# Performance work log

Measured on AMD Instinct MI355X. Metric: run time of the kernel, lower is better.

## Reference

```python
import jax, jax.numpy as jnp
from jax import lax
import numpy as np

B, N, T = 16, 1024, 12
H_DIM, D_FF, NHEADS = 64, 256, 4
SDIM, DDIM, WDIM = 32, 16, 15
D_IN = 1 + SDIM + DDIM + WDIM  # 64


def setup_inputs() -> dict:
    key = jax.random.key(0)
    ks = jax.random.split(key, 32)
    def p(k, shape, s=0.05):
        return jax.random.normal(k, shape, dtype=jnp.float32) * s
    h = H_DIM
    inp = {
        'flow': jax.random.normal(ks[0], (B, N, T), dtype=jnp.float32),
        'day_idx': jax.random.randint(ks[1], (B, N, T), 0, 288),
        'week_idx': jax.random.randint(ks[2], (B, N, T), 0, 7),
        'spatial_emb': p(ks[3], (N, SDIM)),
        'daily_emb': p(ks[4], (288, DDIM)),
        'weekly_emb': p(ks[5], (7, WDIM)),
        'gfs_fc_w': p(ks[6], (h, D_IN)), 'gfs_fc_b': jnp.zeros(h),
        'glu_w': p(ks[7], (2 * h, h)), 'glu_b': jnp.zeros(2 * h),
        'gc_weight': p(ks[8], (h, h)),
        'gc_A': p(ks[9], (N, N), 0.02), 'gc_A2': p(ks[10], (N, N), 0.02),
        'ds_init_w': p(ks[11], (2 * h, h, 1, 3)), 'ds_init_b': jnp.zeros(2 * h),
        'ds_p1m_w': p(ks[12], (h, h, 1, 3)), 'ds_p1m_b': jnp.zeros(h),
        'ds_p1g_w': p(ks[13], (h, h, 1, 3)), 'ds_p1g_b': jnp.zeros(h),
        'ds_p2m_w': p(ks[14], (h, h, 1, 3)), 'ds_p2m_b': jnp.zeros(h),
        'ds_p2g_w': p(ks[15], (h, h, 1, 3)), 'ds_p2g_b': jnp.zeros(h),
        'ds_fc_w': p(ks[16], (h, 2 * h)), 'ds_fc_b': jnp.zeros(h),
        'wq': p(ks[17], (h, h)), 'bq': jnp.zeros(h),
        'wk': p(ks[18], (h, h)), 'bk': jnp.zeros(h),
        'wv': p(ks[19], (h, h)), 'bv': jnp.zeros(h),
        'wo': p(ks[20], (h, h)), 'bo': jnp.zeros(h),
        'ff1_w': p(ks[21], (D_FF, h)), 'ff1_b': jnp.zeros(D_FF),
        'ff2_w': p(ks[22], (h, D_FF)), 'ff2_b': jnp.zeros(h),
        'ln1_g': jnp.ones(h), 'ln1_b': jnp.zeros(h),
        'ln2_g': jnp.ones(h), 'ln2_b': jnp.zeros(h),
        'cl_w': p(ks[23], (T,)), 'cl_b': jnp.zeros(()),
    }
    return inp


def _ln(x, g, b):
    m = jnp.mean(x, -1, keepdims=True)
    v = jnp.mean(jnp.square(x - m), -1, keepdims=True)
    return (x - m) * lax.rsqrt(v + 1e-5) * g + b


def _conv1xk(x, w, b):
    # x: [B, C, N, T], w: [O, I, 1, 3], padding (0,1) along time
    y = lax.conv_general_dilated(x, w, (1, 1), ((0, 0), (1, 1)),
                                 dimension_numbers=('NCHW', 'OIHW', 'NCHW'))
    return y + b[None, :, None, None]


def reference(flow, day_idx, week_idx, spatial_emb, daily_emb, weekly_emb,
              gfs_fc_w, gfs_fc_b, glu_w, glu_b, gc_weight, gc_A, gc_A2,
              ds_init_w, ds_init_b, ds_p1m_w, ds_p1m_b, ds_p1g_w, ds_p1g_b,
              ds_p2m_w, ds_p2m_b, ds_p2g_w, ds_p2g_b, ds_fc_w, ds_fc_b,
              wq, bq, wk, bk, wv, bv, wo, bo, ff1_w, ff1_b, ff2_w, ff2_b,
              ln1_g, ln1_b, ln2_g, ln2_b, cl_w, cl_b):
    h = H_DIM
    # --- InfoEmb: concat flow + spatial + daily + weekly embeddings ---
    sp = jnp.broadcast_to(spatial_emb[None, :, None, :], (B, N, T, SDIM))
    x = jnp.concatenate([flow[..., None], sp, daily_emb[day_idx], weekly_emb[week_idx]], -1)  # [B,N,T,64]
    # --- GFS: 1x1 conv + GLU (channels == last dim) ---
    x = x @ gfs_fc_w.T + gfs_fc_b
    g = x @ glu_w.T + glu_b
    lhs, rhs = g[..., :h], g[..., h:]
    x = lhs * jax.nn.sigmoid(rhs)  # [B,N,T,h]
    # --- TASTGC: adaptive spatial graph conv with two learned adjacencies ---
    A1 = jax.nn.softmax(jax.nn.relu(gc_A), axis=1)
    A2 = jax.nn.softmax(jax.nn.relu(gc_A2), axis=1)
    hs = jnp.einsum('mn,bntd->bmtd', A1, x) + jnp.einsum('mn,bntd->bmtd', A2, x)
    x = jax.nn.relu(jnp.einsum('bntd,de->bnte', hs, gc_weight))  # [B,N,T,h]
    # --- DSFIN: dual-path gated temporal conv ---
    xd = jnp.transpose(x, (0, 3, 1, 2))  # [B,h,N,T]
    x_init = _conv1xk(xd, ds_init_w, ds_init_b)  # [B,2h,N,T]
    p1, p2 = x_init[:, :h], x_init[:, h:]
    p1o = _conv1xk(p1, ds_p1m_w, ds_p1m_b) * jax.nn.sigmoid(_conv1xk(p1, ds_p1g_w, ds_p1g_b))
    p2o = _conv1xk(p2, ds_p2m_w, ds_p2m_b) * jax.nn.sigmoid(_conv1xk(p2, ds_p2g_w, ds_p2g_b))
    fused = jax.nn.relu(jnp.concatenate([p1o, p2o], 1) + x_init)  # [B,2h,N,T]
    fused = jnp.transpose(fused, (0, 2, 3, 1))  # [B,N,T,2h]
    x = fused @ ds_fc_w.T + ds_fc_b  # [B,N,T,h]
    # --- EncoderLayer: multi-head attention along time per node ---
    dk = h // NHEADS
    y = x.reshape(B * N, T, h)
    q = (y @ wq.T + bq).reshape(B * N, T, NHEADS, dk)
    k = (y @ wk.T + bk).reshape(B * N, T, NHEADS, dk)
    v = (y @ wv.T + bv).reshape(B * N, T, NHEADS, dk)
    scores = jnp.einsum('blhd,bshd->bhls', q, k) / jnp.sqrt(jnp.float32(dk))
    attn = jax.nn.softmax(scores, -1)
    o = jnp.einsum('bhls,bshd->blhd', attn, v).reshape(B * N, T, h)
    y1 = _ln(y + (o @ wo.T + bo), ln1_g, ln1_b)
    ff = jax.nn.relu(y1 @ ff1_w.T + ff1_b) @ ff2_w.T + ff2_b
    y2 = _ln(y1 + ff, ln2_g, ln2_b).reshape(B, N, T, h)
    # --- CongestionLearn: symmetric sigmoid node-node gate from flow ---
    f = jax.nn.relu(flow @ cl_w + cl_b)  # [B,N]
    m = jnp.mean(f, 0)  # [N]
    fuse = jax.nn.sigmoid((m[:, None] + m[None, :]) * 0.5)  # [N,N]
    out = jnp.einsum('mn,bntd->bmtd', fuse, y2)  # [B,N,T,h]
    return out
```

## Files before the change

### kernel.cpp

```cpp
#include <hip/hip_runtime.h>
#include <hip/hip_bf16.h>
#include <cstdint>

#define B_ 16
#define N_ 1024
#define T_ 12
#define HD 64
#define BN_ (B_*N_)
#define BNT (B_*N_*T_)
#define TD (T_*HD)

typedef __attribute__((ext_vector_type(8))) short short8;
typedef __attribute__((ext_vector_type(4))) float f32x4;

#define MFMA16(a,b,c) __builtin_amdgcn_mfma_f32_16x16x32_bf16(a,b,c,0,0,0)

__device__ __forceinline__ float sigmoidf_(float x) { return 1.f / (1.f + __expf(-x)); }

__device__ __forceinline__ unsigned short f2bf(float f) {
  __hip_bfloat16 h = __float2bfloat16(f);
  return __builtin_bit_cast(unsigned short, h);
}
__device__ __forceinline__ unsigned int f2bf2(float lo, float hi) {
  return (unsigned int)f2bf(lo) | ((unsigned int)f2bf(hi) << 16);
}
__device__ __forceinline__ float bf2f(unsigned short h) {
  unsigned int u = ((unsigned int)h) << 16;
  return __uint_as_float(u);
}

__device__ __forceinline__ float blkRedMax(float v, float* red) {
  #pragma unroll
  for (int off = 32; off >= 1; off >>= 1) v = fmaxf(v, __shfl_xor(v, off));
  int w = threadIdx.x >> 6;
  if ((threadIdx.x & 63) == 0) red[w] = v;
  __syncthreads();
  v = fmaxf(fmaxf(red[0], red[1]), fmaxf(red[2], red[3]));
  __syncthreads();
  return v;
}
__device__ __forceinline__ float blkRedSum(float v, float* red) {
  #pragma unroll
  for (int off = 32; off >= 1; off >>= 1) v += __shfl_xor(v, off);
  int w = threadIdx.x >> 6;
  if ((threadIdx.x & 63) == 0) red[w] = v;
  __syncthreads();
  v = red[0] + red[1] + red[2] + red[3];
  __syncthreads();
  return v;
}

__global__ void k_wprep_all(
    const float* __restrict__ w1, const float* __restrict__ w2, const float* __restrict__ gcw,
    const float* __restrict__ wi,
    const float* __restrict__ w1m, const float* __restrict__ w1g,
    const float* __restrict__ w2m, const float* __restrict__ w2g,
    const float* __restrict__ wfc,
    const float* __restrict__ wq, const float* __restrict__ wk,
    const float* __restrict__ wv, const float* __restrict__ wo,
    const float* __restrict__ f1w, const float* __restrict__ f2w,
    unsigned short* __restrict__ wTe, unsigned short* __restrict__ wds,
    unsigned short* __restrict__ wat)
{
  int t = blockIdx.x*256 + threadIdx.x;
  if (t < 4096)        wat[t] = f2bf(wq[t]);
  else if (t < 8192)   wat[t] = f2bf(wk[t-4096]);
  else if (t < 12288)  wat[t] = f2bf(wv[t-8192]);
  else if (t < 16384)  wat[t] = f2bf(wo[t-12288]);
  else if (t < 32768)  wat[t] = f2bf(f1w[t-16384]);
  else                 wat[t] = f2bf(f2w[t-32768]);
  if (t < 4096)       wTe[t] = f2bf(w1[t]);
  else if (t < 12288) wTe[t] = f2bf(w2[t-4096]);
  else if (t < 16384) {
    int r = t - 12288, e = r >> 6, d = r & 63;
    wTe[12288 + e*64 + d] = f2bf(gcw[d*64 + e]);
  }
  if (t < 24576) {
    int o = t / 192, k = t - o*192, tap = k >> 6, i = k & 63;
    wds[o*192 + k] = f2bf(wi[(o*64 + i)*3 + tap]);
  }
  if (t < 12288) {
    int o = t / 192, k = t - o*192, tap = k >> 6, i = k & 63;
    int src = (o*64 + i)*3 + tap;
    wds[24576 + o*192 + k]      = f2bf(w1m[src]);
    wds[24576 + (64+o)*192 + k] = f2bf(w1g[src]);
    wds[49152 + o*192 + k]      = f2bf(w2m[src]);
    wds[49152 + (64+o)*192 + k] = f2bf(w2g[src]);
  }
  if (t < 8192) wds[73728 + t] = f2bf(wfc[t]);
}

__global__ __launch_bounds__(256) void k_embed3(
    const float* __restrict__ flow, const int* __restrict__ day, const int* __restrict__ week,
    const float* __restrict__ semb, const float* __restrict__ demb, const float* __restrict__ wemb,
    const unsigned short* __restrict__ wTe, const float* __restrict__ b1,
    const float* __restrict__ b2,
    unsigned short* __restrict__ outw)
{
  __shared__ unsigned short sEa[128*72];
  __shared__ unsigned short sEb[128*72];
  const unsigned short* W1  = wTe;
  const unsigned short* W2  = wTe + 4096;
  const unsigned short* GcT = wTe + 12288;

  int tid = threadIdx.x, lane = tid & 63, w = tid >> 6;
  int l15 = lane & 15, l4 = lane >> 4;
  int row0 = blockIdx.x * 128;

  for (int i = tid; i < 8192; i += 256) {
    int r = i >> 6, c = i & 63;
    int row = row0 + r;
    int n = (row / T_) & (N_-1);
    float val;
    if (c == 0)      val = flow[row];
    else if (c < 33) val = semb[n*32 + (c-1)];
    else if (c < 49) val = demb[day[row]*16 + (c-33)];
    else             val = wemb[week[row]*15 + (c-49)];
    sEa[r*72 + c] = f2bf(val);
  }
  __syncthreads();

  {
    f32x4 acc[8] = {};
    #pragma unroll
    for (int ks = 0; ks < 2; ++ks) {
      short8 bf = *(const short8*)&W1[(w*16 + l15)*64 + ks*32 + l4*8];
      #pragma unroll
      for (int mt = 0; mt < 8; ++mt) {
        short8 af = *(const short8*)&sEa[(mt*16 + l15)*72 + ks*32 + l4*8];
        acc[mt] = MFMA16(af, bf, acc[mt]);
      }
    }
    float bias = b1[w*16 + l15];
    #pragma unroll
    for (int mt = 0; mt < 8; ++mt)
      #pragma unroll
      for (int r = 0; r < 4; ++r)
        sEb[(mt*16 + l4*4 + r)*72 + w*16 + l15] = f2bf(acc[mt][r] + bias);
  }
  __syncthreads();

  {
    f32x4 alo[8] = {}, ahi[8] = {};
    #pragma unroll
    for (int ks = 0; ks < 2; ++ks) {
      short8 blo = *(const short8*)&W2[(size_t)(w*16 + l15)*64 + ks*32 + l4*8];
      short8 bhi = *(const short8*)&W2[(size_t)(64 + w*16 + l15)*64 + ks*32 + l4*8];
      #pragma unroll
      for (int mt = 0; mt < 8; ++mt) {
        short8 af = *(const short8*)&sEb[(mt*16 + l15)*72 + ks*32 + l4*8];
        alo[mt] = MFMA16(af, blo, alo[mt]);
        ahi[mt] = MFMA16(af, bhi, ahi[mt]);
      }
    }
    float blov = b2[w*16 + l15], bhiv = b2[64 + w*16 + l15];
    #pragma unroll
    for (int mt = 0; mt < 8; ++mt)
      #pragma unroll
      for (int r = 0; r < 4; ++r) {
        float v = (alo[mt][r] + blov) * sigmoidf_(ahi[mt][r] + bhiv);
        sEa[(mt*16 + l4*4 + r)*72 + w*16 + l15] = f2bf(v);
      }
  }
  __syncthreads();

  {
    f32x4 acc[8] = {};
    #pragma unroll
    for (int ks = 0; ks < 2; ++ks) {
      short8 bf = *(const short8*)&GcT[(w*16 + l15)*64 + ks*32 + l4*8];
      #pragma unroll
      for (int mt = 0; mt < 8; ++mt) {
        short8 af = *(const short8*)&sEa[(mt*16 + l15)*72 + ks*32 + l4*8];
        acc[mt] = MFMA16(af, bf, acc[mt]);
      }
    }
    #pragma unroll
    for (int mt = 0; mt < 8; ++mt)
      #pragma unroll
      for (int r = 0; r < 4; ++r)
        outw[(size_t)(row0 + mt*16 + l4*4 + r)*64 + w*16 + l15] = f2bf(acc[mt][r]);
  }
}

__global__ __launch_bounds__(256) void k_aprep(
    const float* __restrict__ A1, const float* __restrict__ A2, unsigned short* __restrict__ Aout)
{
  __shared__ float red[4];
  int m = blockIdx.x, tid = threadIdx.x;
  float mx0, is0, mx1, is1;
  {
    const float* src = A1 + (size_t)m*N_;
    float mx = 0.f;
    for (int i = tid; i < N_; i += 256) mx = fmaxf(mx, fmaxf(src[i], 0.f));
    mx = blkRedMax(mx, red);
    float s = 0.f;
    for (int i = tid; i < N_; i += 256) s += __expf(fmaxf(src[i], 0.f) - mx);
    s = blkRedSum(s, red);
    mx0 = mx; is0 = 1.f / s;
  }
  {
    const float* src = A2 + (size_t)m*N_;
    float mx = 0.f;
    for (int i = tid; i < N_; i += 256) mx = fmaxf(mx, fmaxf(src[i], 0.f));
    mx = blkRedMax(mx, red);
    float s = 0.f;
    for (int i = tid; i < N_; i += 256) s += __expf(fmaxf(src[i], 0.f) - mx);
    s = blkRedSum(s, red);
    mx1 = mx; is1 = 1.f / s;
  }
  const float* s1 = A1 + (size_t)m*N_;
  const float* s2 = A2 + (size_t)m*N_;
  for (int i = tid; i < N_; i += 256) {
    float v1 = __expf(fmaxf(s1[i], 0.f) - mx0) * is0;
    float v2 = __expf(fmaxf(s2[i], 0.f) - mx1) * is1;
    Aout[(size_t)m*N_ + i] = f2bf(v1 + v2);
  }
}

template<int RELU, int OB16>
__global__ __launch_bounds__(256) void k_gemm_mfma(
    const unsigned short* __restrict__ A, const unsigned short* __restrict__ X,
    void* __restrict__ C, int K, int P)
{
  __shared__ unsigned short sA[128*40];
  __shared__ unsigned short sB[128*40];
  int tid = threadIdx.x, lane = tid & 63, wid = tid >> 6;
  int M = gridDim.y * 128;
  int b = blockIdx.z;
  const unsigned short* Xb = X + (size_t)b*K*P;
  int m0 = blockIdx.y*128, p0 = blockIdx.x*128;
  int wr = wid >> 1, wc = wid & 1;

  f32x4 acc[4][4] = {};

  for (int k0 = 0; k0 < K; k0 += 32) {
    #pragma unroll
    for (int pass = 0; pass < 2; ++pass) {
      int r = (tid >> 2) + 64*pass, kk = (tid & 3)*8;
      short8 v = *(const short8*)&A[(size_t)(m0+r)*K + k0 + kk];
      *(short8*)&sA[r*40 + kk] = v;
    }
    #pragma unroll
    for (int pass = 0; pass < 4; ++pass) {
      int p  = (tid & 63) + 64*(pass & 1);
      int k4 = (tid >> 6)*4 + 16*(pass >> 1);
      ushort4 h;
      h.x = Xb[(size_t)(k0+k4+0)*P + p0 + p];
      h.y = Xb[(size_t)(k0+k4+1)*P + p0 + p];
      h.z = Xb[(size_t)(k0+k4+2)*P + p0 + p];
      h.w = Xb[(size_t)(k0+k4+3)*P + p0 + p];
      *(ushort4*)&sB[p*40 + k4] = h;
    }
    __syncthreads();
    short8 af[4], bf[4];
    #pragma unroll
    for (int f = 0; f < 4; ++f) {
      af[f] = *(const short8*)&sA[(wr*64 + f*16 + (lane & 15))*40 + (lane >> 4)*8];
      bf[f] = *(const short8*)&sB[(wc*64 + f*16 + (lane & 15))*40 + (lane >> 4)*8];
    }
    #pragma unroll
    for (int fm = 0; fm < 4; ++fm)
      #pragma unroll
      for (int fn = 0; fn < 4; ++fn)
        acc[fm][fn] = MFMA16(af[fm], bf[fn], acc[fm][fn]);
    __syncthreads();
  }
  #pragma unroll
  for (int fm = 0; fm < 4; ++fm) {
    int row = m0 + wr*64 + fm*16 + (lane >> 4)*4;
    #pragma unroll
    for (int fn = 0; fn < 4; ++fn) {
      int col = p0 + wc*64 + fn*16 + (lane & 15);
      #pragma unroll
      for (int r = 0; r < 4; ++r) {
        float v = acc[fm][fn][r];
        if (RELU) v = fmaxf(v, 0.f);
        if (OB16) {
          unsigned short* Cb = (unsigned short*)C + (size_t)b*M*P;
          Cb[(size_t)(row + r)*P + col] = f2bf(v);
        } else {
          float* Cb = (float*)C + (size_t)b*M*P;
          Cb[(size_t)(row + r)*P + col] = v;
        }
      }
    }
  }
}

__global__ __launch_bounds__(256) void k_ds3(
    const unsigned short* xds,
    const unsigned short* __restrict__ Wall,
    const float* __restrict__ bi,
    const float* __restrict__ b1m, const float* __restrict__ b1g,
    const float* __restrict__ b2m, const float* __restrict__ b2g,
    const float* __restrict__ bfc,
    unsigned short* outg)
{
  __shared__ unsigned short smem[36352];
  unsigned short* X_lds  = smem;
  unsigned short* xi_lds = smem + 8064;
  unsigned short* fu_lds = smem + 23296;
  const unsigned short* WiB  = Wall;
  const unsigned short* Wg1B = Wall + 24576;
  const unsigned short* Wg2B = Wall + 49152;
  const unsigned short* WfB  = Wall + 73728;

  int tid = threadIdx.x, lane = tid & 63, wid = tid >> 6;
  int l15 = lane & 15, l4 = lane >> 4;
  int bn0 = blockIdx.x * 8;

  for (int i = tid; i < 8*2*72; i += 256) {
    int g = i / 144, r = i - g*144;
    int tp = (r < 72) ? 0 : 13, c = (r < 72) ? r : r - 72;
    X_lds[(g*14 + tp)*72 + c] = 0;
  }
  for (int i = tid; i < 8*2*136; i += 256) {
    int g = i / 272, r = i - g*272;
    int tp = (r < 136) ? 0 : 13, c = (r < 136) ? r : r - 136;
    xi_lds[(g*14 + tp)*136 + c] = 0;
  }
  for (int i = tid; i < 768; i += 256) {
    int g = i / 96, rem = i - g*96, t = rem >> 3, i8 = rem & 7;
    short8 v = *(const short8*)&xds[(size_t)(bn0+g)*768 + t*64 + i8*8];
    *(short8*)&X_lds[(g*14 + t + 1)*72 + i8*8] = v;
  }
  __syncthreads();

  int ga[6], ta[6];
  #pragma unroll
  for (int mt = 0; mt < 6; ++mt) {
    int r = mt*16 + l15;
    ga[mt] = r / 12; ta[mt] = r - ga[mt]*12;
  }

  {
    f32x4 acc1[6][2] = {};
    int nb = wid*2;
    #pragma unroll
    for (int ks = 0; ks < 6; ++ks) {
      int tap = ks >> 1, i0 = (ks & 1)*32;
      short8 af[6];
      #pragma unroll
      for (int mt = 0; mt < 6; ++mt)
        af[mt] = *(const short8*)&X_lds[(ga[mt]*14 + ta[mt] + tap)*72 + i0 + l4*8];
      short8 bf0 = *(const short8*)&WiB[(size_t)((nb  )*16 + l15)*192 + ks*32 + l4*8];
      short8 bf1 = *(const short8*)&WiB[(size_t)((nb+1)*16 + l15)*192 + ks*32 + l4*8];
      #pragma unroll
      for (int mt = 0; mt < 6; ++mt) {
        acc1[mt][0] = MFMA16(af[mt], bf0, acc1[mt][0]);
        acc1[mt][1] = MFMA16(af[mt], bf1, acc1[mt][1]);
      }
    }
    #pragma unroll
    for (int nn = 0; nn < 2; ++nn) {
      int o = (nb+nn)*16 + l15;
      float bv = bi[o];
      #pragma unroll
      for (int mt = 0; mt < 6; ++mt) {
        #pragma unroll
        for (int reg = 0; reg < 4; ++reg) {
          int r = mt*16 + l4*4 + reg;
          int g = r / 12, t = r - g*12;
          xi_lds[(g*14 + t + 1)*136 + o] = f2bf(acc1[mt][nn][reg] + bv);
        }
      }
    }
  }
  __syncthreads();

  #pragma unroll
  for (int h = 0; h < 2; ++h) {
    const unsigned short* Wg = h ? Wg2B : Wg1B;
    f32x4 am[6] = {}, ag[6] = {};
    #pragma unroll
    for (int ks = 0; ks < 6; ++ks) {
      int tap = ks >> 1, i0 = (ks & 1)*32;
      short8 af[6];
      #pragma unroll
      for (int mt = 0; mt < 6; ++mt)
        af[mt] = *(const short8*)&xi_lds[(ga[mt]*14 + ta[mt] + tap)*136 + h*64 + i0 + l4*8];
      short8 bm = *(const short8*)&Wg[(size_t)(wid*16 + l15)*192 + ks*32 + l4*8];
      short8 bg = *(const short8*)&Wg[(size_t)((wid+4)*16 + l15)*192 + ks*32 + l4*8];
      #pragma unroll
      for (int mt = 0; mt < 6; ++mt) {
        am[mt] = MFMA16(af[mt], bm, am[mt]);
        ag[mt] = MFMA16(af[mt], bg, ag[mt]);
      }
    }
    int o = wid*16 + l15;
    float bmv = (h ? b2m : b1m)[o];
    float bgv = (h ? b2g : b1g)[o];
    #pragma unroll
    for (int mt = 0; mt < 6; ++mt) {
      #pragma unroll
      for (int reg = 0; reg < 4; ++reg) {
        int r = mt*16 + l4*4 + reg;
        int g = r / 12, t = r - g*12;
        float pm = am[mt][reg] + bmv;
        float pg = ag[mt][reg] + bgv;
        float po = pm * sigmoidf_(pg);
        float xi = bf2f(xi_lds[(g*14 + t + 1)*136 + h*64 + o]);
        fu_lds[r*136 + h*64 + o] = f2bf(fmaxf(po + xi, 0.f));
      }
    }
  }
  __syncthreads();

  {
    f32x4 a3[6] = {};
    #pragma unroll
    for (int ks = 0; ks < 4; ++ks) {
      short8 af = *(const short8*)&WfB[(size_t)(wid*16 + l15)*128 + ks*32 + l4*8];
      #pragma unroll
      for (int nt = 0; nt < 6; ++nt) {
        short8 bf = *(const short8*)&fu_lds[(nt*16 + l15)*136 + ks*32 + l4*8];
        a3[nt] = MFMA16(af, bf, a3[nt]);
      }
    }
    int e0 = wid*16 + l4*4;
    float4 bb = *(const float4*)&bfc[e0];
    #pragma unroll
    for (int nt = 0; nt < 6; ++nt) {
      uint2 vv;
      vv.x = f2bf2(a3[nt][0] + bb.x, a3[nt][1] + bb.y);
      vv.y = f2bf2(a3[nt][2] + bb.z, a3[nt][3] + bb.w);
      *(uint2*)&outg[((size_t)(bn0 + ga[nt])*12 + ta[nt])*64 + e0] = vv;
    }
  }
}

__global__ __launch_bounds__(512, 4) void k_attn5(
    const unsigned short* __restrict__ xg,
    const unsigned short* __restrict__ Wat,
    const float* __restrict__ bq, const float* __restrict__ bk, const float* __restrict__ bv,
    const float* __restrict__ bo,
    const float* __restrict__ f1b, const float* __restrict__ f2b,
    const float* __restrict__ g1, const float* __restrict__ be1,
    const float* __restrict__ g2, const float* __restrict__ be2,
    unsigned short* __restrict__ outg)
{
  __shared__ unsigned short su[26112];
  __shared__ unsigned short partb[2][4][96];
  unsigned short* Ybuf = su;
  unsigned short* Qkv  = su + 6912;
  unsigned short* Hb   = su + 6912;

  const unsigned short* Wqkv = Wat;
  const unsigned short* Wo   = Wat + 12288;
  const unsigned short* F1   = Wat + 16384;
  const unsigned short* F2   = Wat + 32768;

  int tid = threadIdx.x, lane = tid & 63, w = tid >> 6;
  int l15 = lane & 15, l4 = lane >> 4;
  int wn = w & 3, wm = w >> 2;
  size_t base = (size_t)blockIdx.x * 8 * 768;

  for (int i = tid; i < 768; i += 512) {
    int r = i >> 3, c = i & 7;
    *(short8*)&Ybuf[r*72 + c*8] = *(const short8*)&xg[base + r*64 + c*8];
  }
  __syncthreads();

  {
    f32x4 acc[3][3] = {};
    #pragma unroll
    for (int ks = 0; ks < 2; ++ks) {
      short8 af[3];
      #pragma unroll
      for (int mi = 0; mi < 3; ++mi)
        af[mi] = *(const short8*)&Ybuf[((wm*3+mi)*16 + l15)*72 + ks*32 + l4*8];
      #pragma unroll
      for (int ni = 0; ni < 3; ++ni) {
        short8 bf = *(const short8*)&Wqkv[(size_t)((wn*3+ni)*16 + l15)*64 + ks*32 + l4*8];
        #pragma unroll
        for (int mi = 0; mi < 3; ++mi)
          acc[mi][ni] = MFMA16(af[mi], bf, acc[mi][ni]);
      }
    }
    #pragma unroll
    for (int ni = 0; ni < 3; ++ni) {
      int col = (wn*3+ni)*16 + l15;
      float bias = col < 64 ? bq[col] : (col < 128 ? bk[col-64] : bv[col-128]);
      #pragma unroll
      for (int mi = 0; mi < 3; ++mi)
        #pragma unroll
        for (int r = 0; r < 4; ++r)
          Qkv[((wm*3+mi)*16 + l4*4 + r)*200 + col] = f2bf(acc[mi][ni][r] + bias);
    }
  }
  __syncthreads();

  {
    int rb = w*12;
    int src0 = (l15 + 32*l4) & 63;
    int src1 = (src0 + 16) & 63;
    #pragma unroll
    for (int h = 0; h < 4; ++h) {
      short8 kf = {}, qf = {};
      if (l4 < 2) {
        kf = *(const short8*)&Qkv[(rb + l15)*200 + 64 + h*16 + l4*8];
        qf = *(const short8*)&Qkv[(rb + l15)*200 +      h*16 + l4*8];
      }
      f32x4 sc = {};
      sc = MFMA16(kf, qf, sc);
      float e[4]; float mx = -3e38f;
      #pragma unroll
      for (int r = 0; r < 4; ++r) {
        float v = (l4 == 3) ? -3e38f : sc[r]*0.25f;
        e[r] = v; mx = fmaxf(mx, v);
      }
      mx = fmaxf(mx, __shfl_xor(mx, 16));
      mx = fmaxf(mx, __shfl_xor(mx, 32));
      float s = 0.f;
      #pragma unroll
      for (int r = 0; r < 4; ++r) { e[r] = __expf(e[r] - mx); s += e[r]; }
      s += __shfl_xor(s, 16); s += __shfl_xor(s, 32);
      float inv = 1.f/s;
      int pk0 = (int)f2bf2(e[0]*inv, e[1]*inv);
      int pk1 = (int)f2bf2(e[2]*inv, e[3]*inv);
      int a0 = __shfl(pk0, src0), b0 = __shfl(pk1, src0);
      int c0 = __shfl(pk0, src1), d0 = __shfl(pk1, src1);
      short8 aaf = {};
      if (l4 < 2) {
        uint4 u = make_uint4((unsigned)a0, (unsigned)b0, (unsigned)c0, (unsigned)d0);
        aaf = __builtin_bit_cast(short8, u);
      }
      short8 vf = {};
      if (l4 < 2) {
        #pragma unroll
        for (int j = 0; j < 8; ++j) {
          int s_ = l4*8 + j;
          vf[j] = (s_ < 12) ? (short)Qkv[(rb + s_)*200 + 128 + h*16 + l15] : (short)0;
        }
      }
      f32x4 o = {};
      o = MFMA16(aaf, vf, o);
      if (l4 < 3) {
        #pragma unroll
        for (int r = 0; r < 4; ++r)
          Qkv[(rb + l4*4 + r)*200 + h*16 + l15] = f2bf(o[r]);
      }
    }
  }
  __syncthreads();

  {
    f32x4 zacc[3] = {};
    #pragma unroll
    for (int ks = 0; ks < 2; ++ks) {
      short8 bf = *(const short8*)&Wo[(size_t)(wn*16 + l15)*64 + ks*32 + l4*8];
      #pragma unroll
      for (int mi = 0; mi < 3; ++mi) {
        short8 af = *(const short8*)&Qkv[((wm*3+mi)*16 + l15)*200 + ks*32 + l4*8];
        zacc[mi] = MFMA16(af, bf, zacc[mi]);
      }
    }
    int col = wn*16 + l15;
    float bias = bo[col];
    #pragma unroll
    for (int mi = 0; mi < 3; ++mi)
      #pragma unroll
      for (int r = 0; r < 4; ++r) {
        int row = (wm*3+mi)*16 + l4*4 + r;
        float z = zacc[mi][r] + bias + bf2f(Ybuf[row*72 + col]);
        zacc[mi][r] = z;
        float s1 = z, s2 = z*z;
        #pragma unroll
        for (int off = 1; off <= 8; off <<= 1) { s1 += __shfl_xor(s1, off); s2 += __shfl_xor(s2, off); }
        if (l15 == 0) { partb[0][wn][row] = f2bf(s1); partb[1][wn][row] = f2bf(s2); }
      }
    __syncthreads();
    if (tid < 96) {
      float s = bf2f(partb[0][0][tid])+bf2f(partb[0][1][tid])+bf2f(partb[0][2][tid])+bf2f(partb[0][3][tid]);
      float q = bf2f(partb[1][0][tid])+bf2f(partb[1][1][tid])+bf2f(partb[1][2][tid])+bf2f(partb[1][3][tid]);
      float mu = s * (1.f/64.f);
      float var = q * (1.f/64.f) - mu*mu;
      partb[0][0][tid] = f2bf(mu); partb[1][0][tid] = f2bf(rsqrtf(var + 1e-5f));
    }
    __syncthreads();
    float gv = g1[col], bvv = be1[col];
    #pragma unroll
    for (int mi = 0; mi < 3; ++mi)
      #pragma unroll
      for (int r = 0; r < 4; ++r) {
        int row = (wm*3+mi)*16 + l4*4 + r;
        float mu = bf2f(partb[0][0][row]), rs = bf2f(partb[1][0][row]);
        Ybuf[row*72 + col] = f2bf((zacc[mi][r] - mu) * rs * gv + bvv);
      }
  }
  __syncthreads();

  {
    f32x4 acc2[3] = {};
    #pragma unroll
    for (int fh = 0; fh < 2; ++fh) {
      {
        f32x4 acc[3][2] = {};
        #pragma unroll
        for (int ks = 0; ks < 2; ++ks) {
          short8 af[3];
          #pragma unroll
          for (int mi = 0; mi < 3; ++mi)
            af[mi] = *(const short8*)&Ybuf[((wm*3+mi)*16 + l15)*72 + ks*32 + l4*8];
          #pragma unroll
          for (int i = 0; i < 2; ++i) {
            int frow = fh*128 + (wn*2+i)*16 + l15;
            short8 bf = *(const short8*)&F1[(size_t)frow*64 + ks*32 + l4*8];
            #pragma unroll
            for (int mi = 0; mi < 3; ++mi)
              acc[mi][i] = MFMA16(af[mi], bf, acc[mi][i]);
          }
        }
        #pragma unroll
        for (int i = 0; i < 2; ++i) {
          int cl = (wn*2+i)*16 + l15;
          float bias = f1b[fh*128 + cl];
          #pragma unroll
          for (int mi = 0; mi < 3; ++mi)
            #pragma unroll
            for (int r = 0; r < 4; ++r)
              Hb[((wm*3+mi)*16 + l4*4 + r)*136 + cl] = f2bf(fmaxf(acc[mi][i][r] + bias, 0.f));
        }
      }
      __syncthreads();
      #pragma unroll
      for (int k2 = 0; k2 < 4; ++k2) {
        short8 bf = *(const short8*)&F2[(size_t)(wn*16 + l15)*256 + fh*128 + k2*32 + l4*8];
        #pragma unroll
        for (int mi = 0; mi < 3; ++mi) {
          short8 af = *(const short8*)&Hb[((wm*3+mi)*16 + l15)*136 + k2*32 + l4*8];
          acc2[mi] = MFMA16(af, bf, acc2[mi]);
        }
      }
      if (fh == 0) __syncthreads();
    }
    int col = wn*16 + l15;
    float bias = f2b[col];
    #pragma unroll
    for (int mi = 0; mi < 3; ++mi)
      #pragma unroll
      for (int r = 0; r < 4; ++r) {
        int row = (wm*3+mi)*16 + l4*4 + r;
        float z = acc2[mi][r] + bias + bf2f(Ybuf[row*72 + col]);
        acc2[mi][r] = z;
        float s1 = z, s2 = z*z;
        #pragma unroll
        for (int off = 1; off <= 8; off <<= 1) { s1 += __shfl_xor(s1, off); s2 += __shfl_xor(s2, off); }
        if (l15 == 0) { partb[0][wn][row] = f2bf(s1); partb[1][wn][row] = f2bf(s2); }
      }
    __syncthreads();
    if (tid < 96) {
      float s = bf2f(partb[0][0][tid])+bf2f(partb[0][1][tid])+bf2f(partb[0][2][tid])+bf2f(partb[0][3][tid]);
      float q = bf2f(partb[1][0][tid])+bf2f(partb[1][1][tid])+bf2f(partb[1][2][tid])+bf2f(partb[1][3][tid]);
      float mu = s * (1.f/64.f);
      float var = q * (1.f/64.f) - mu*mu;
      partb[0][0][tid] = f2bf(mu); partb[1][0][tid] = f2bf(rsqrtf(var + 1e-5f));
    }
    __syncthreads();
    float gv = g2[col], bvv = be2[col];
    #pragma unroll
    for (int mi = 0; mi < 3; ++mi)
      #pragma unroll
      for (int r = 0; r < 4; ++r) {
        int row = (wm*3+mi)*16 + l4*4 + r;
        float mu = bf2f(partb[0][0][row]), rs = bf2f(partb[1][0][row]);
        outg[base + row*64 + col] = f2bf((acc2[mi][r] - mu) * rs * gv + bvv);
      }
  }
}

__global__ void k_mvec(const float* __restrict__ flow, const float* __restrict__ clw,
                       const float* __restrict__ clb, float* __restrict__ mv)
{
  int n = blockIdx.x*blockDim.x + threadIdx.x;
  if (n < N_) {
    float s = 0.f;
    float bias = clb[0];
    for (int b = 0; b < B_; ++b) {
      const float* f = flow + ((size_t)b*N_ + n)*T_;
      float acc = bias;
      #pragma unroll
      for (int t = 0; t < T_; ++t) acc += f[t]*clw[t];
      s += fmaxf(acc, 0.f);
    }
    mv[n] = s * (1.f/16.f);
  }
}

__global__ void k_fusemat(const float* __restrict__ mv, unsigned short* __restrict__ F)
{
  int idx = blockIdx.x*256 + threadIdx.x;
  int m = idx >> 10, n = idx & 1023;
  float x = 0.5f*(mv[m] + mv[n]);
  F[idx] = f2bf(1.f/(1.f + __expf(-x)));
}

extern "C" void kernel_launch(void* const* d_in, const int* in_sizes, int n_in,
                              void* d_out, int out_size, void* d_ws, size_t ws_size,
                              hipStream_t stream)
{
  const float* flow = (const float*)d_in[0];
  const int*   day  = (const int*)d_in[1];
  const int*   week = (const int*)d_in[2];
  const float* semb = (const float*)d_in[3];
  const float* demb = (const float*)d_in[4];
  const float* wemb = (const float*)d_in[5];
  const float* gfsw = (const float*)d_in[6];
  const float* gfsb = (const float*)d_in[7];
  const float* gluw = (const float*)d_in[8];
  const float* glub = (const float*)d_in[9];
  const float* gcw  = (const float*)d_in[10];
  const float* gcA  = (const float*)d_in[11];
  const float* gcA2 = (const float*)d_in[12];
  const float* wi   = (const float*)d_in[13];
  const float* bi   = (const float*)d_in[14];
  const float* w1m  = (const float*)d_in[15];
  const float* b1m  = (const float*)d_in[16];
  const float* w1g  = (const float*)d_in[17];
  const float* b1g  = (const float*)d_in[18];
  const float* w2m  = (const float*)d_in[19];
  const float* b2m  = (const float*)d_in[20];
  const float* w2g  = (const float*)d_in[21];
  const float* b2g  = (const float*)d_in[22];
  const float* wfc  = (const float*)d_in[23];
  const float* bfc  = (const float*)d_in[24];
  const float* wq   = (const float*)d_in[25];
  const float* bq   = (const float*)d_in[26];
  const float* wk   = (const float*)d_in[27];
  const float* bk   = (const float*)d_in[28];
  const float* wv   = (const float*)d_in[29];
  const float* bv   = (const float*)d_in[30];
  const float* wo   = (const float*)d_in[31];
  const float* bo   = (const float*)d_in[32];
  const float* f1w  = (const float*)d_in[33];
  const float* f1b  = (const float*)d_in[34];
  const float* f2w  = (const float*)d_in[35];
  const float* f2b  = (const float*)d_in[36];
  const float* g1   = (const float*)d_in[37];
  const float* be1  = (const float*)d_in[38];
  const float* g2   = (const float*)d_in[39];
  const float* be2  = (const float*)d_in[40];
  const float* clw  = (const float*)d_in[41];
  const float* clb  = (const float*)d_in[42];

  float* out = (float*)d_out;
  char* ws = (char*)d_ws;
  unsigned short* Amat = (unsigned short*)ws;
  float* mv  = (float*)(ws + (size_t)2*1024*1024);
  unsigned short* wTe = (unsigned short*)(ws + (size_t)2*1024*1024 + 64*1024);
  unsigned short* wds = (unsigned short*)(ws + (size_t)2*1024*1024 + 128*1024);
  unsigned short* wat = (unsigned short*)(ws + (size_t)2*1024*1024 + 320*1024);
  unsigned short* xw  = (unsigned short*)(ws + (size_t)3*1024*1024);
  unsigned short* xds = (unsigned short*)(ws + (size_t)28*1024*1024);

  k_wprep_all<<<192, 256, 0, stream>>>(gfsw, gluw, gcw,
                                       wi, w1m, w1g, w2m, w2g, wfc,
                                       wq, wk, wv, wo, f1w, f2w,
                                       wTe, wds, wat);
  k_embed3<<<BNT/128, 256, 0, stream>>>(flow, day, week, semb, demb, wemb,
                                        wTe, gfsb, glub, xw);
  k_aprep<<<N_, 256, 0, stream>>>(gcA, gcA2, Amat);
  dim3 gg(TD/128, N_/128, B_);
  k_gemm_mfma<1,1><<<gg, 256, 0, stream>>>(Amat, xw, xds, N_, TD);
  k_ds3<<<BN_/8, 256, 0, stream>>>(xds, wds, bi, b1m, b1g, b2m, b2g, bfc, xds);
  k_attn5<<<BN_/8, 512, 0, stream>>>(xds, wat, bq, bk, bv, bo, f1b, f2b,
                                     g1, be1, g2, be2, xw);
  k_mvec<<<N_/256, 256, 0, stream>>>(flow, clw, clb, mv);
  k_fusemat<<<(N_*N_)/256, 256, 0, stream>>>(mv, Amat);
  k_gemm_mfma<0,0><<<gg, 256, 0, stream>>>(Amat, xw, out, N_, TD);
}
```

Measured before the change: 329.1 us.

## Give each wave its own node in attention kernel, removing block barriers

The attention/FFN kernel now assigns one node (12 time steps, padded to 16 rows) per wave, each with a private LDS slice, instead of splitting 8 nodes' 96 rows across 8 waves in a 2x4 tile grid. All __syncthreads and the cross-wave LayerNorm partial-sum exchange are gone, and LayerNorm stats are reduced in registers with shuffles. The trade-off is that a quarter of each 16-row MFMA tile is padding, each wave reloads every weight fragment itself, per-wave accumulators grow (12 QKV tiles, 8 FF1 tiles), and the min-blocks-per-CU launch bound is dropped.

New measurement: 418.7 us. 27.2% more time.

```diff
diff --git a/kernel.cpp b/kernel.cpp
--- a/kernel.cpp
+++ b/kernel.cpp
@@ -430,7 +430,7 @@
   }
 }
 
-__global__ __launch_bounds__(512, 4) void k_attn5(
+__global__ __launch_bounds__(512) void k_attn6(
     const unsigned short* __restrict__ xg,
     const unsigned short* __restrict__ Wat,
     const float* __restrict__ bq, const float* __restrict__ bk, const float* __restrict__ bv,
@@ -440,67 +440,56 @@
     const float* __restrict__ g2, const float* __restrict__ be2,
     unsigned short* __restrict__ outg)
 {
-  __shared__ unsigned short su[26112];
-  __shared__ unsigned short partb[2][4][96];
-  unsigned short* Ybuf = su;
-  unsigned short* Qkv  = su + 6912;
-  unsigned short* Hb   = su + 6912;
+  __shared__ unsigned short su[34816];
+  int tid = threadIdx.x, lane = tid & 63, w = tid >> 6;
+  int l15 = lane & 15, l4 = lane >> 4;
+  unsigned short* Ybuf = su + w*4352;
+  unsigned short* Qkv  = Ybuf + 1152;
+  unsigned short* Hb   = Qkv;
 
   const unsigned short* Wqkv = Wat;
   const unsigned short* Wo   = Wat + 12288;
   const unsigned short* F1   = Wat + 16384;
   const unsigned short* F2   = Wat + 32768;
 
-  int tid = threadIdx.x, lane = tid & 63, w = tid >> 6;
-  int l15 = lane & 15, l4 = lane >> 4;
-  int wn = w & 3, wm = w >> 2;
-  size_t base = (size_t)blockIdx.x * 8 * 768;
-
-  for (int i = tid; i < 768; i += 512) {
+  int bn = blockIdx.x*8 + w;
+  size_t base = (size_t)bn * 768;
+
+  for (int i = lane; i < 96; i += 64) {
     int r = i >> 3, c = i & 7;
     *(short8*)&Ybuf[r*72 + c*8] = *(const short8*)&xg[base + r*64 + c*8];
   }
-  __syncthreads();
-
-  {
-    f32x4 acc[3][3] = {};
+
+  {
+    f32x4 acc[12] = {};
     #pragma unroll
     for (int ks = 0; ks < 2; ++ks) {
-      short8 af[3];
-      #pragma unroll
-      for (int mi = 0; mi < 3; ++mi)
-        af[mi] = *(const short8*)&Ybuf[((wm*3+mi)*16 + l15)*72 + ks*32 + l4*8];
-      #pragma unroll
-      for (int ni = 0; ni < 3; ++ni) {
-        short8 bf = *(const short8*)&Wqkv[(size_t)((wn*3+ni)*16 + l15)*64 + ks*32 + l4*8];
-        #pragma unroll
-        for (int mi = 0; mi < 3; ++mi)
-          acc[mi][ni] = MFMA16(af[mi], bf, acc[mi][ni]);
-      }
-    }
-    #pragma unroll
-    for (int ni = 0; ni < 3; ++ni) {
-      int col = (wn*3+ni)*16 + l15;
+      short8 af = *(const short8*)&Ybuf[l15*72 + ks*32 + l4*8];
+      #pragma unroll
+      for (int ni = 0; ni < 12; ++ni) {
+        short8 bf = *(const short8*)&Wqkv[(size_t)(ni*16 + l15)*64 + ks*32 + l4*8];
+        acc[ni] = MFMA16(af, bf, acc[ni]);
+      }
+    }
+    #pragma unroll
+    for (int ni = 0; ni < 12; ++ni) {
+      int col = ni*16 + l15;
       float bias = col < 64 ? bq[col] : (col < 128 ? bk[col-64] : bv[col-128]);
       #pragma unroll
-      for (int mi = 0; mi < 3; ++mi)
-        #pragma unroll
-        for (int r = 0; r < 4; ++r)
-          Qkv[((wm*3+mi)*16 + l4*4 + r)*200 + col] = f2bf(acc[mi][ni][r] + bias);
-    }
-  }
-  __syncthreads();
-
-  {
-    int rb = w*12;
+      for (int r = 0; r < 4; ++r)
+        Qkv[(l4*4 + r)*200 + col] = f2bf(acc[ni][r] + bias);
+    }
+  }
+
+  {
     int src0 = (l15 + 32*l4) & 63;
     int src1 = (src0 + 16) & 63;
     #pragma unroll
     for (int h = 0; h < 4; ++h) {
       short8 kf = {}, qf = {};
       if (l4 < 2) {
-        kf = *(const short8*)&Qkv[(rb + l15)*200 + 64 + h*16 + l4*8];
-        qf = *(const short8*)&Qkv[(rb + l15)*200 +      h*16 + l4*8];
+        kf = *(const short8*)&Qkv[l15*200 + 64 + h*16 + l4*8];
+        qf = *(const short8*)&Qkv[l15*200 +      h*16 + l4*8];
       }
       f32x4 sc = {};
       sc = MFMA16(kf, qf, sc);
@@ -531,7 +520,7 @@
         #pragma unroll
         for (int j = 0; j < 8; ++j) {
           int s_ = l4*8 + j;
-          vf[j] = (s_ < 12) ? (short)Qkv[(rb + s_)*200 + 128 + h*16 + l15] : (short)0;
+          vf[j] = (s_ < 12) ? (short)Qkv[s_*200 + 128 + h*16 + l15] : (short)0;
         }
       }
       f32x4 o = {};
@@ -539,134 +528,115 @@
       if (l4 < 3) {
         #pragma unroll
         for (int r = 0; r < 4; ++r)
-          Qkv[(rb + l4*4 + r)*200 + h*16 + l15] = f2bf(o[r]);
-      }
-    }
-  }
-  __syncthreads();
-
-  {
-    f32x4 zacc[3] = {};
+          Qkv[(l4*4 + r)*200 + h*16 + l15] = f2bf(o[r]);
+      }
+    }
+  }
+
+  {
+    f32x4 zacc[4] = {};
     #pragma unroll
     for (int ks = 0; ks < 2; ++ks) {
-      short8 bf = *(const short8*)&Wo[(size_t)(wn*16 + l15)*64 + ks*32 + l4*8];
-      #pragma unroll
-      for (int mi = 0; mi < 3; ++mi) {
-        short8 af = *(const short8*)&Qkv[((wm*3+mi)*16 + l15)*200 + ks*32 + l4*8];
-        zacc[mi] = MFMA16(af, bf, zacc[mi]);
-      }
-    }
-    int col = wn*16 + l15;
-    float bias = bo[col];
-    #pragma unroll
-    for (int mi = 0; mi < 3; ++mi)
+      short8 af = *(const short8*)&Qkv[l15*200 + ks*32 + l4*8];
+      #pragma unroll
+      for (int ni = 0; ni < 4; ++ni) {
+        short8 bf = *(const short8*)&Wo[(size_t)(ni*16 + l15)*64 + ks*32 + l4*8];
+        zacc[ni] = MFMA16(af, bf, zacc[ni]);
+      }
+    }
+    float z[4][4];
+    float gv[4], bvv[4];
+    #pragma unroll
+    for (int ni = 0; ni < 4; ++ni) {
+      int col = ni*16 + l15;
+      float bias = bo[col];
+      gv[ni] = g1[col]; bvv[ni] = be1[col];
       #pragma unroll
       for (int r = 0; r < 4; ++r) {
-        int row = (wm*3+mi)*16 + l4*4 + r;
-        float z = zacc[mi][r] + bias + bf2f(Ybuf[row*72 + col]);
-        zacc[mi][r] = z;
-        float s1 = z, s2 = z*z;
+        int row = l4*4 + r;
+        z[ni][r] = zacc[ni][r] + bias + bf2f(Ybuf[row*72 + col]);
+      }
+    }
+    #pragma unroll
+    for (int r = 0; r < 4; ++r) {
+      float s1 = z[0][r] + z[1][r] + z[2][r] + z[3][r];
+      float s2 = z[0][r]*z[0][r] + z[1][r]*z[1][r] + z[2][r]*z[2][r] + z[3][r]*z[3][r];
+      #pragma unroll
+      for (int off = 1; off <= 8; off <<= 1) { s1 += __shfl_xor(s1, off); s2 += __shfl_xor(s2, off); }
+      float mu = s1 * (1.f/64.f);
+      float var = s2 * (1.f/64.f) - mu*mu;
+      float rs = rsqrtf(var + 1e-5f);
+      int row = l4*4 + r;
+      #pragma unroll
+      for (int ni = 0; ni < 4; ++ni)
+        Ybuf[row*72 + ni*16 + l15] = f2bf((z[ni][r] - mu) * rs * gv[ni] + bvv[ni]);
+    }
+  }
+
+  f32x4 acc2[4] = {};
+  #pragma unroll
+  for (int fh = 0; fh < 2; ++fh) {
+    {
+      f32x4 a1[8] = {};
+      #pragma unroll
+      for (int ks = 0; ks < 2; ++ks) {
+        short8 af = *(const short8*)&Ybuf[l15*72 + ks*32 + l4*8];
         #pragma unroll
-        for (int off = 1; off <= 8; off <<= 1) { s1 += __shfl_xor(s1, off); s2 += __shfl_xor(s2, off); }
-        if (l15 == 0) { partb[0][wn][row] = f2bf(s1); partb[1][wn][row] = f2bf(s2); }
-      }
-    __syncthreads();
-    if (tid < 96) {
-      float s = bf2f(partb[0][0][tid])+bf2f(partb[0][1][tid])+bf2f(partb[0][2][tid])+bf2f(partb[0][3][tid]);
-      float q = bf2f(partb[1][0][tid])+bf2f(partb[1][1][tid])+bf2f(partb[1][2][tid])+bf2f(partb[1][3][tid]);
-      float mu = s * (1.f/64.f);
-      float var = q * (1.f/64.f) - mu*mu;
-      partb[0][0][tid] = f2bf(mu); partb[1][0][tid] = f2bf(rsqrtf(var + 1e-5f));
-    }
-    __syncthreads();
-    float gv = g1[col], bvv = be1[col];
-    #pragma unroll
-    for (int mi = 0; mi < 3; ++mi)
+        for (int i = 0; i < 8; ++i) {
+          short8 bf = *(const short8*)&F1[(size_t)(fh*128 + i*16 + l15)*64 + ks*32 + l4*8];
+          a1[i] = MFMA16(af, bf, a1[i]);
+        }
+      }
+      #pragma unroll
+      for (int i = 0; i < 8; ++i) {
+        int cl = i*16 + l15;
+        float bias = f1b[fh*128 + cl];
+        #pragma unroll
+        for (int r = 0; r < 4; ++r)
+          Hb[(l4*4 + r)*136 + cl] = f2bf(fmaxf(a1[i][r] + bias, 0.f));
+      }
+    }
+    #pragma unroll
+    for (int k2 = 0; k2 < 4; ++k2) {
+      short8 af = *(const short8*)&Hb[l15*136 + k2*32 + l4*8];
+      #pragma unroll
+      for (int ni = 0; ni < 4; ++ni) {
+        short8 bf = *(const short8*)&F2[(size_t)(ni*16 + l15)*256 + fh*128 + k2*32 + l4*8];
+        acc2[ni] = MFMA16(af, bf, acc2[ni]);
+      }
+    }
+  }
+
+  {
+    float z[4][4];
+    float gv[4], bvv[4];
+    #pragma unroll
+    for (int ni = 0; ni < 4; ++ni) {
+      int col = ni*16 + l15;
+      float bias = f2b[col];
+      gv[ni] = g2[col]; bvv[ni] = be2[col];
       #pragma unroll
       for (int r = 0; r < 4; ++r) {
-        int row = (wm*3+mi)*16 + l4*4 + r;
-        float mu = bf2f(partb[0][0][row]), rs = bf2f(partb[1][0][row]);
-        Ybuf[row*72 + col] = f2bf((zacc[mi][r] - mu) * rs * gv + bvv);
-      }
-  }
-  __syncthreads();
-
-  {
-    f32x4 acc2[3] = {};
-    #pragma unroll
-    for (int fh = 0; fh < 2; ++fh) {
-      {
-        f32x4 acc[3][2] = {};
+        int row = l4*4 + r;
+        z[ni][r] = acc2[ni][r] + bias + bf2f(Ybuf[row*72 + col]);
+      }
+    }
+    #pragma unroll
+    for (int r = 0; r < 4; ++r) {
+      float s1 = z[0][r] + z[1][r] + z[2][r] + z[3][r];
+      float s2 = z[0][r]*z[0][r] + z[1][r]*z[1][r] + z[2][r]*z[2][r] + z[3][r]*z[3][r];
+      #pragma unroll
+      for (int off = 1; off <= 8; off <<= 1) { s1 += __shfl_xor(s1, off); s2 += __shfl_xor(s2, off); }
+      float mu = s1 * (1.f/64.f);
+      float var = s2 * (1.f/64.f) - mu*mu;
+      float rs = rsqrtf(var + 1e-5f);
+      int row = l4*4 + r;
+      if (l4 < 3) {
         #pragma unroll
-        for (int ks = 0; ks < 2; ++ks) {
-          short8 af[3];
-          #pragma unroll
-          for (int mi = 0; mi < 3; ++mi)
-            af[mi] = *(const short8*)&Ybuf[((wm*3+mi)*16 + l15)*72 + ks*32 + l4*8];
-          #pragma unroll
-          for (int i = 0; i < 2; ++i) {
-            int frow = fh*128 + (wn*2+i)*16 + l15;
-            short8 bf = *(const short8*)&F1[(size_t)frow*64 + ks*32 + l4*8];
-            #pragma unroll
-            for (int mi = 0; mi < 3; ++mi)
-              acc[mi][i] = MFMA16(af[mi], bf, acc[mi][i]);
-          }
-        }
-        #pragma unroll
-        for (int i = 0; i < 2; ++i) {
-          int cl = (wn*2+i)*16 + l15;
-          float bias = f1b[fh*128 + cl];
-          #pragma unroll
-          for (int mi = 0; mi < 3; ++mi)
-            #pragma unroll
-            for (int r = 0; r < 4; ++r)
-              Hb[((wm*3+mi)*16 + l4*4 + r)*136 + cl] = f2bf(fmaxf(acc[mi][i][r] + bias, 0.f));
-        }
-      }
-      __syncthreads();
-      #pragma unroll
-      for (int k2 = 0; k2 < 4; ++k2) {
-        short8 bf = *(const short8*)&F2[(size_t)(wn*16 + l15)*256 + fh*128 + k2*32 + l4*8];
-        #pragma unroll
-        for (int mi = 0; mi < 3; ++mi) {
-          short8 af = *(const short8*)&Hb[((wm*3+mi)*16 + l15)*136 + k2*32 + l4*8];
-          acc2[mi] = MFMA16(af, bf, acc2[mi]);
-        }
-      }
-      if (fh == 0) __syncthreads();
-    }
-    int col = wn*16 + l15;
-    float bias = f2b[col];
-    #pragma unroll
-    for (int mi = 0; mi < 3; ++mi)
-      #pragma unroll
-      for (int r = 0; r < 4; ++r) {
-        int row = (wm*3+mi)*16 + l4*4 + r;
-        float z = acc2[mi][r] + bias + bf2f(Ybuf[row*72 + col]);
-        acc2[mi][r] = z;
-        float s1 = z, s2 = z*z;
-        #pragma unroll
-        for (int off = 1; off <= 8; off <<= 1) { s1 += __shfl_xor(s1, off); s2 += __shfl_xor(s2, off); }
-        if (l15 == 0) { partb[0][wn][row] = f2bf(s1); partb[1][wn][row] = f2bf(s2); }
-      }
-    __syncthreads();
-    if (tid < 96) {
-      float s = bf2f(partb[0][0][tid])+bf2f(partb[0][1][tid])+bf2f(partb[0][2][tid])+bf2f(partb[0][3][tid]);
-      float q = bf2f(partb[1][0][tid])+bf2f(partb[1][1][tid])+bf2f(partb[1][2][tid])+bf2f(partb[1][3][tid]);
-      float mu = s * (1.f/64.f);
-      float var = q * (1.f/64.f) - mu*mu;
-      partb[0][0][tid] = f2bf(mu); partb[1][0][tid] = f2bf(rsqrtf(var + 1e-5f));
-    }
-    __syncthreads();
-    float gv = g2[col], bvv = be2[col];
-    #pragma unroll
-    for (int mi = 0; mi < 3; ++mi)
-      #pragma unroll
-      for (int r = 0; r < 4; ++r) {
-        int row = (wm*3+mi)*16 + l4*4 + r;
-        float mu = bf2f(partb[0][0][row]), rs = bf2f(partb[1][0][row]);
-        outg[base + row*64 + col] = f2bf((acc2[mi][r] - mu) * rs * gv + bvv);
-      }
+        for (int ni = 0; ni < 4; ++ni)
+          outg[base + row*64 + ni*16 + l15] = f2bf((z[ni][r] - mu) * rs * gv[ni] + bvv[ni]);
+      }
+    }
   }
 }
 
@@ -764,7 +734,7 @@
   dim3 gg(TD/128, N_/128, B_);
   k_gemm_mfma<1,1><<<gg, 256, 0, stream>>>(Amat, xw, xds, N_, TD);
   k_ds3<<<BN_/8, 256, 0, stream>>>(xds, wds, bi, b1m, b1g, b2m, b2g, bfc, xds);
-  k_attn5<<<BN_/8, 512, 0, stream>>>(xds, wat, bq, bk, bv, bo, f1b, f2b,
+  k_attn6<<<BN_/8, 512, 0, stream>>>(xds, wat, bq, bk, bv, bo, f1b, f2b,
                                      g1, be1, g2, be2, xw);
   k_mvec<<<N_/256, 256, 0, stream>>>(flow, clw, clb, mv);
   k_fusemat<<<(N_*N_)/256, 256, 0, stream>>>(mv, Amat);
```

## Pre-transpose GEMM operand and stage tiles via direct global-to-LDS loads

Applied to the files above, without the earlier changes.

Adds a tiled transpose kernel so the GEMM B operand is K-contiguous, then replaces the register-staged tile loads in both node-mixing GEMMs with global_load_lds 16-byte direct-to-LDS copies into unpadded tiles. The aim is to remove the strided 2-byte gathers and the VGPR round trip when filling shared memory. In exchange it adds two extra transpose passes over a 25MB buffer and drops the LDS padding, which may cause bank conflicts on the fragment reads.

Result: no change. 333.8 us (+1.4%).

```diff
diff --git a/kernel.cpp b/kernel.cpp
--- a/kernel.cpp
+++ b/kernel.cpp
@@ -14,6 +14,10 @@
 typedef __attribute__((ext_vector_type(4))) float f32x4;
 
 #define MFMA16(a,b,c) __builtin_amdgcn_mfma_f32_16x16x32_bf16(a,b,c,0,0,0)
+
+#define GLD16(g, l) __builtin_amdgcn_global_load_lds( \
+    (const __attribute__((address_space(1))) unsigned int*)(g), \
+    (__attribute__((address_space(3))) unsigned int*)(l), 16, 0, 0)
 
 __device__ __forceinline__ float sigmoidf_(float x) { return 1.f / (1.f + __expf(-x)); }
 
@@ -218,46 +222,61 @@
   }
 }
 
+__global__ __launch_bounds__(256) void k_transp(
+    const unsigned short* __restrict__ X, unsigned short* __restrict__ XT)
+{
+  __shared__ unsigned short tl[64*65];
+  int b = blockIdx.z;
+  int p0 = blockIdx.x*64, n0 = blockIdx.y*64;
+  const unsigned short* Xb = X + (size_t)b*1024*768;
+  unsigned short* XTb = XT + (size_t)b*768*1024;
+  int t = threadIdx.x;
+  int lr = t >> 6, lc = t & 63;
+  #pragma unroll
+  for (int it = 0; it < 16; ++it) {
+    int r = it*4 + lr;
+    tl[lc*65 + r] = Xb[(size_t)(n0+r)*768 + p0 + lc];
+  }
+  __syncthreads();
+  #pragma unroll
+  for (int it = 0; it < 16; ++it) {
+    int p = it*4 + lr;
+    XTb[(size_t)(p0+p)*1024 + n0 + lc] = tl[p*65 + lc];
+  }
+}
+
 template<int RELU, int OB16>
-__global__ __launch_bounds__(256) void k_gemm_mfma(
-    const unsigned short* __restrict__ A, const unsigned short* __restrict__ X,
+__global__ __launch_bounds__(256) void k_gemm_glds(
+    const unsigned short* __restrict__ A, const unsigned short* __restrict__ XT,
     void* __restrict__ C, int K, int P)
 {
-  __shared__ unsigned short sA[128*40];
-  __shared__ unsigned short sB[128*40];
+  __shared__ unsigned short sA[128*32];
+  __shared__ unsigned short sB[128*32];
   int tid = threadIdx.x, lane = tid & 63, wid = tid >> 6;
   int M = gridDim.y * 128;
   int b = blockIdx.z;
-  const unsigned short* Xb = X + (size_t)b*K*P;
   int m0 = blockIdx.y*128, p0 = blockIdx.x*128;
   int wr = wid >> 1, wc = wid & 1;
+  int l15 = lane & 15, l4 = lane >> 4;
+
+  const unsigned short* Ag = A  + (size_t)(m0 + wid*32 + (lane>>2))*K + (lane&3)*8;
+  const unsigned short* Bg = XT + ((size_t)b*P + p0 + wid*32 + (lane>>2))*K + (lane&3)*8;
+  unsigned short* lA = sA + wid*1024;
+  unsigned short* lB = sB + wid*1024;
 
   f32x4 acc[4][4] = {};
 
   for (int k0 = 0; k0 < K; k0 += 32) {
-    #pragma unroll
-    for (int pass = 0; pass < 2; ++pass) {
-      int r = (tid >> 2) + 64*pass, kk = (tid & 3)*8;
-      short8 v = *(const short8*)&A[(size_t)(m0+r)*K + k0 + kk];
-      *(short8*)&sA[r*40 + kk] = v;
-    }
-    #pragma unroll
-    for (int pass = 0; pass < 4; ++pass) {
-      int p  = (tid & 63) + 64*(pass & 1);
-      int k4 = (tid >> 6)*4 + 16*(pass >> 1);
-      ushort4 h;
-      h.x = Xb[(size_t)(k0+k4+0)*P + p0 + p];
-      h.y = Xb[(size_t)(k0+k4+1)*P + p0 + p];
-      h.z = Xb[(size_t)(k0+k4+2)*P + p0 + p];
-      h.w = Xb[(size_t)(k0+k4+3)*P + p0 + p];
-      *(ushort4*)&sB[p*40 + k4] = h;
-    }
+    GLD16(Ag + k0,                 lA);
+    GLD16(Ag + k0 + (size_t)16*K,  lA + 512);
+    GLD16(Bg + k0,                 lB);
+    GLD16(Bg + k0 + (size_t)16*K,  lB + 512);
     __syncthreads();
     short8 af[4], bf[4];
     #pragma unroll
     for (int f = 0; f < 4; ++f) {
-      af[f] = *(const short8*)&sA[(wr*64 + f*16 + (lane & 15))*40 + (lane >> 4)*8];
-      bf[f] = *(const short8*)&sB[(wc*64 + f*16 + (lane & 15))*40 + (lane >> 4)*8];
+      af[f] = *(const short8*)&sA[(wr*64 + f*16 + l15)*32 + l4*8];
+      bf[f] = *(const short8*)&sB[(wc*64 + f*16 + l15)*32 + l4*8];
     }
     #pragma unroll
     for (int fm = 0; fm < 4; ++fm)
@@ -268,10 +287,10 @@
   }
   #pragma unroll
   for (int fm = 0; fm < 4; ++fm) {
-    int row = m0 + wr*64 + fm*16 + (lane >> 4)*4;
+    int row = m0 + wr*64 + fm*16 + l4*4;
     #pragma unroll
     for (int fn = 0; fn < 4; ++fn) {
-      int col = p0 + wc*64 + fn*16 + (lane & 15);
+      int col = p0 + wc*64 + fn*16 + l15;
       #pragma unroll
       for (int r = 0; r < 4; ++r) {
         float v = acc[fm][fn][r];
@@ -751,22 +770,25 @@
   unsigned short* wTe = (unsigned short*)(ws + (size_t)2*1024*1024 + 64*1024);
   unsigned short* wds = (unsigned short*)(ws + (size_t)2*1024*1024 + 128*1024);
   unsigned short* wat = (unsigned short*)(ws + (size_t)2*1024*1024 + 320*1024);
-  unsigned short* xw  = (unsigned short*)(ws + (size_t)3*1024*1024);
-  unsigned short* xds = (unsigned short*)(ws + (size_t)28*1024*1024);
+  unsigned short* bufA = (unsigned short*)(ws + (size_t)3*1024*1024);
+  unsigned short* bufB = (unsigned short*)(ws + (size_t)28*1024*1024);
 
   k_wprep_all<<<192, 256, 0, stream>>>(gfsw, gluw, gcw,
                                        wi, w1m, w1g, w2m, w2g, wfc,
                                        wq, wk, wv, wo, f1w, f2w,
                                        wTe, wds, wat);
   k_embed3<<<BNT/128, 256, 0, stream>>>(flow, day, week, semb, demb, wemb,
-                                        wTe, gfsb, glub, xw);
+                                        wTe, gfsb, glub, bufA);
   k_aprep<<<N_, 256, 0, stream>>>(gcA, gcA2, Amat);
+  dim3 gt(12, 16, B_);
+  k_transp<<<gt, 256, 0, stream>>>(bufA, bufB);
   dim3 gg(TD/128, N_/128, B_);
-  k_gemm_mfma<1,1><<<gg, 256, 0, stream>>>(Amat, xw, xds, N_, TD);
-  k_ds3<<<BN_/8, 256, 0, stream>>>(xds, wds, bi, b1m, b1g, b2m, b2g, bfc, xds);
-  k_attn5<<<BN_/8, 512, 0, stream>>>(xds, wat, bq, bk, bv, bo, f1b, f2b,
-                                     g1, be1, g2, be2, xw);
+  k_gemm_glds<1,1><<<gg, 256, 0, stream>>>(Amat, bufB, bufA, N_, TD);
+  k_ds3<<<BN_/8, 256, 0, stream>>>(bufA, wds, bi, b1m, b1g, b2m, b2g, bfc, bufA);
+  k_attn5<<<BN_/8, 512, 0, stream>>>(bufA, wat, bq, bk, bv, bo, f1b, f2b,
+                                     g1, be1, g2, be2, bufB);
+  k_transp<<<gt, 256, 0, stream>>>(bufB, bufA);
   k_mvec<<<N_/256, 256, 0, stream>>>(flow, clw, clb, mv);
   k_fusemat<<<(N_*N_)/256, 256, 0, stream>>>(mv, Amat);
-  k_gemm_mfma<0,0><<<gg, 256, 0, stream>>>(Amat, xw, out, N_, TD);
-}
+  k_gemm_glds<0,0><<<gg, 256, 0, stream>>>(Amat, bufA, out, N_, TD);
+}
```
